# Performance work log

Measured on AMD Instinct MI355X. Metric: run time of the kernel, lower is better.

Reference implementation:

```python
import jax, jax.numpy as jnp
import numpy as np


def setup_inputs() -> dict:
    key = jax.random.key(0)
    k1, k2, k3 = jax.random.split(key, 3)
    n, num_dim, classes = 65536, 1024, 1000
    inputs = jax.random.normal(k1, (n, num_dim), dtype=jnp.float32)
    targets = jax.random.randint(k2, (n,), 0, classes, dtype=jnp.int64)
    class_weight = jax.random.normal(k3, (classes, num_dim), dtype=jnp.float32)
    return {"inputs": inputs, "targets": targets, "classes": classes, "class_weight": class_weight}


def reference(inputs, targets, classes, class_weight):
    # Per-class mean (segment mean) for classes present in the batch;
    # absent classes fall back to the corresponding class_weight row.
    sums = jax.ops.segment_sum(inputs, targets, num_segments=classes)  # [classes, dim]
    counts = jax.ops.segment_sum(jnp.ones((inputs.shape[0],), inputs.dtype), targets, num_segments=classes)  # [classes]
    present = counts > 0
    means = sums / jnp.maximum(counts, 1.0)[:, None]
    centers = jnp.where(present[:, None], means, class_weight)
    return centers
```

## Files before the change

### kernel.cpp

```cpp
#include <hip/hip_runtime.h>


typedef float floatx4 __attribute__((ext_vector_type(4)));

__global__ void zero_kernel(int* __restrict__ p, int n) {
    int i = blockIdx.x * blockDim.x + threadIdx.x;
    if (i < n) p[i] = 0;
}

__global__ void count_kernel(const int* __restrict__ targets, int* __restrict__ counts, int n) {
    int i = blockIdx.x * blockDim.x + threadIdx.x;
    if (i < n) atomicAdd(&counts[targets[i]], 1);
}

__global__ void scan_kernel(const int* __restrict__ counts, int* __restrict__ offsets, int c) {
    __shared__ int buf[2][1024];
    int tid = threadIdx.x;
    int v = (tid < c) ? counts[tid] : 0;
    buf[0][tid] = v;
    __syncthreads();
    int src = 0;
    for (int d = 1; d < 1024; d <<= 1) {
        int x = buf[src][tid];
        if (tid >= d) x += buf[src][tid - d];
        buf[src ^ 1][tid] = x;
        src ^= 1;
        __syncthreads();
    }
    if (tid < c) offsets[tid] = buf[src][tid] - v;
}

__global__ void scatter_kernel(const int* __restrict__ targets,
                               const int* __restrict__ offsets,
                               int* __restrict__ cursors,
                               int* __restrict__ binned, int n) {
    int i = blockIdx.x * blockDim.x + threadIdx.x;
    if (i < n) {
        int t = targets[i];
        int pos = atomicAdd(&cursors[t], 1);
        binned[offsets[t] + pos] = i;
    }
}

__global__ void gather_kernel(const floatx4* __restrict__ in4,
                              const int* __restrict__ counts,
                              const int* __restrict__ offsets,
                              const int* __restrict__ binned,
                              floatx4* __restrict__ part4, int d4) {
    int b = blockIdx.x;
    int c = b >> 1, half = b & 1;
    int cnt = counts[c];
    if (cnt == 0) return;
    int mid = (cnt + 1) >> 1;
    int begin = half ? mid : 0;
    int end   = half ? cnt : mid;
    int off = offsets[c] + begin;
    int m = end - begin;
    int tid = threadIdx.x;

    __shared__ int rows[1024];
    floatx4 a0 = {0,0,0,0}, a1 = {0,0,0,0}, a2 = {0,0,0,0}, a3 = {0,0,0,0};
    floatx4 a4 = {0,0,0,0}, a5 = {0,0,0,0}, a6 = {0,0,0,0}, a7 = {0,0,0,0};

    for (int base = 0; base < m; base += 1024) {
        int mm = min(m - base, 1024);
        __syncthreads();
        for (int j = tid; j < mm; j += blockDim.x) rows[j] = binned[off + base + j];
        __syncthreads();
        int j = 0;
        for (; j + 7 < mm; j += 8) {
            int r0 = rows[j],   r1 = rows[j+1], r2 = rows[j+2], r3 = rows[j+3];
            int r4 = rows[j+4], r5 = rows[j+5], r6 = rows[j+6], r7 = rows[j+7];
            a0 += __builtin_nontemporal_load(&in4[(size_t)r0 * d4 + tid]);
            a1 += __builtin_nontemporal_load(&in4[(size_t)r1 * d4 + tid]);
            a2 += __builtin_nontemporal_load(&in4[(size_t)r2 * d4 + tid]);
            a3 += __builtin_nontemporal_load(&in4[(size_t)r3 * d4 + tid]);
            a4 += __builtin_nontemporal_load(&in4[(size_t)r4 * d4 + tid]);
            a5 += __builtin_nontemporal_load(&in4[(size_t)r5 * d4 + tid]);
            a6 += __builtin_nontemporal_load(&in4[(size_t)r6 * d4 + tid]);
            a7 += __builtin_nontemporal_load(&in4[(size_t)r7 * d4 + tid]);
        }
        for (; j < mm; ++j)
            a0 += __builtin_nontemporal_load(&in4[(size_t)rows[j] * d4 + tid]);
    }
    floatx4 s = ((a0 + a1) + (a2 + a3)) + ((a4 + a5) + (a6 + a7));
    part4[(size_t)b * d4 + tid] = s;
}

__global__ void finalize_kernel(const floatx4* __restrict__ part4,
                                const floatx4* __restrict__ w4,
                                const int* __restrict__ counts,
                                floatx4* __restrict__ out4, int d4) {
    int c = blockIdx.x;
    int tid = threadIdx.x;
    int cnt = counts[c];
    size_t o = (size_t)c * d4 + tid;
    floatx4 r;
    if (cnt > 0) {
        floatx4 s = part4[(size_t)(c << 1) * d4 + tid]
                  + part4[(size_t)((c << 1) | 1) * d4 + tid];
        r = s * (1.0f / (float)cnt);
    } else {
        r = w4[o];
    }
    out4[o] = r;
}

extern "C" void kernel_launch(void* const* d_in, const int* in_sizes, int n_in,
                              void* d_out, int out_size, void* d_ws, size_t ws_size,
                              hipStream_t stream) {
    const float* inputs = (const float*)d_in[0];
    const int* targets  = (const int*)d_in[1];
    const float* weight = (const float*)d_in[3];

    const int N = in_sizes[1];
    const int D = in_sizes[0] / N;
    const int C = in_sizes[3] / D;
    const int D4 = D / 4;

    int* counts  = (int*)d_ws;
    int* cursors = counts + C;
    int* offsets = cursors + C;
    int* binned  = offsets + C;
    float* part  = (float*)(binned + N);

    zero_kernel<<<(2 * C + 255) / 256, 256, 0, stream>>>(counts, 2 * C);

    count_kernel<<<(N + 255) / 256, 256, 0, stream>>>(targets, counts, N);

    scan_kernel<<<1, 1024, 0, stream>>>(counts, offsets, C);

    scatter_kernel<<<(N + 255) / 256, 256, 0, stream>>>(targets, offsets, cursors, binned, N);

    gather_kernel<<<2 * C, D4, 0, stream>>>(
        (const floatx4*)inputs, counts, offsets, binned, (floatx4*)part, D4);

    finalize_kernel<<<C, D4, 0, stream>>>(
        (const floatx4*)part, (const floatx4*)weight, counts, (floatx4*)d_out, D4);
}
```

Before: 391.5 us.

## Fuse histogram and scan into one block, split gather into four per class

Replaces the zero, count and scan kernels with a single one-block kernel that builds the class histogram in shared memory, scans it, and writes the counts, offsets and starting cursors. The scatter kernel now writes directly at an atomically advanced cursor. The gather splits each class across four blocks instead of two to raise parallelism, and it uses normal loads instead of nontemporal ones. The single-block histogram serializes a pass over 65536 targets on one CU, which adds latency that may offset the two launches it removes.

```diff
diff --git a/kernel.cpp b/kernel.cpp
--- a/kernel.cpp
+++ b/kernel.cpp
@@ -3,20 +3,20 @@
 
 typedef float floatx4 __attribute__((ext_vector_type(4)));
 
-__global__ void zero_kernel(int* __restrict__ p, int n) {
-    int i = blockIdx.x * blockDim.x + threadIdx.x;
-    if (i < n) p[i] = 0;
-}
+#define SPLIT 4
 
-__global__ void count_kernel(const int* __restrict__ targets, int* __restrict__ counts, int n) {
-    int i = blockIdx.x * blockDim.x + threadIdx.x;
-    if (i < n) atomicAdd(&counts[targets[i]], 1);
-}
-
-__global__ void scan_kernel(const int* __restrict__ counts, int* __restrict__ offsets, int c) {
+__global__ void hist_scan_kernel(const int* __restrict__ targets, int n, int c,
+                                 int* __restrict__ counts,
+                                 int* __restrict__ offsets,
+                                 int* __restrict__ cursors) {
+    __shared__ int h[1024];
     __shared__ int buf[2][1024];
     int tid = threadIdx.x;
-    int v = (tid < c) ? counts[tid] : 0;
+    h[tid] = 0;
+    __syncthreads();
+    for (int i = tid; i < n; i += 1024) atomicAdd(&h[targets[i]], 1);
+    __syncthreads();
+    int v = h[tid];
     buf[0][tid] = v;
     __syncthreads();
     int src = 0;
@@ -27,18 +27,21 @@
         src ^= 1;
         __syncthreads();
     }
-    if (tid < c) offsets[tid] = buf[src][tid] - v;
+    if (tid < c) {
+        int excl = buf[src][tid] - v;
+        counts[tid]  = v;
+        offsets[tid] = excl;
+        cursors[tid] = excl;
+    }
 }
 
 __global__ void scatter_kernel(const int* __restrict__ targets,
-                               const int* __restrict__ offsets,
                                int* __restrict__ cursors,
                                int* __restrict__ binned, int n) {
     int i = blockIdx.x * blockDim.x + threadIdx.x;
     if (i < n) {
-        int t = targets[i];
-        int pos = atomicAdd(&cursors[t], 1);
-        binned[offsets[t] + pos] = i;
+        int pos = atomicAdd(&cursors[targets[i]], 1);
+        binned[pos] = i;
     }
 }
 
@@ -48,12 +51,11 @@
                               const int* __restrict__ binned,
                               floatx4* __restrict__ part4, int d4) {
     int b = blockIdx.x;
-    int c = b >> 1, half = b & 1;
+    int c = b >> 2, q = b & 3;
     int cnt = counts[c];
     if (cnt == 0) return;
-    int mid = (cnt + 1) >> 1;
-    int begin = half ? mid : 0;
-    int end   = half ? cnt : mid;
+    int begin = (cnt * q) >> 2;
+    int end   = (cnt * (q + 1)) >> 2;
     int off = offsets[c] + begin;
     int m = end - begin;
     int tid = threadIdx.x;
@@ -71,17 +73,17 @@
         for (; j + 7 < mm; j += 8) {
             int r0 = rows[j],   r1 = rows[j+1], r2 = rows[j+2], r3 = rows[j+3];
             int r4 = rows[j+4], r5 = rows[j+5], r6 = rows[j+6], r7 = rows[j+7];
-            a0 += __builtin_nontemporal_load(&in4[(size_t)r0 * d4 + tid]);
-            a1 += __builtin_nontemporal_load(&in4[(size_t)r1 * d4 + tid]);
-            a2 += __builtin_nontemporal_load(&in4[(size_t)r2 * d4 + tid]);
-            a3 += __builtin_nontemporal_load(&in4[(size_t)r3 * d4 + tid]);
-            a4 += __builtin_nontemporal_load(&in4[(size_t)r4 * d4 + tid]);
-            a5 += __builtin_nontemporal_load(&in4[(size_t)r5 * d4 + tid]);
-            a6 += __builtin_nontemporal_load(&in4[(size_t)r6 * d4 + tid]);
-            a7 += __builtin_nontemporal_load(&in4[(size_t)r7 * d4 + tid]);
+            a0 += in4[(size_t)r0 * d4 + tid];
+            a1 += in4[(size_t)r1 * d4 + tid];
+            a2 += in4[(size_t)r2 * d4 + tid];
+            a3 += in4[(size_t)r3 * d4 + tid];
+            a4 += in4[(size_t)r4 * d4 + tid];
+            a5 += in4[(size_t)r5 * d4 + tid];
+            a6 += in4[(size_t)r6 * d4 + tid];
+            a7 += in4[(size_t)r7 * d4 + tid];
         }
         for (; j < mm; ++j)
-            a0 += __builtin_nontemporal_load(&in4[(size_t)rows[j] * d4 + tid]);
+            a0 += in4[(size_t)rows[j] * d4 + tid];
     }
     floatx4 s = ((a0 + a1) + (a2 + a3)) + ((a4 + a5) + (a6 + a7));
     part4[(size_t)b * d4 + tid] = s;
@@ -97,8 +99,9 @@
     size_t o = (size_t)c * d4 + tid;
     floatx4 r;
     if (cnt > 0) {
-        floatx4 s = part4[(size_t)(c << 1) * d4 + tid]
-                  + part4[(size_t)((c << 1) | 1) * d4 + tid];
+        size_t pb = (size_t)(c << 2) * d4 + tid;
+        floatx4 s = (part4[pb] + part4[pb + d4])
+                  + (part4[pb + 2 * d4] + part4[pb + 3 * d4]);
         r = s * (1.0f / (float)cnt);
     } else {
         r = w4[o];
@@ -124,15 +127,11 @@
     int* binned  = offsets + C;
     float* part  = (float*)(binned + N);
 
-    zero_kernel<<<(2 * C + 255) / 256, 256, 0, stream>>>(counts, 2 * C);
+    hist_scan_kernel<<<1, 1024, 0, stream>>>(targets, N, C, counts, offsets, cursors);
 
-    count_kernel<<<(N + 255) / 256, 256, 0, stream>>>(targets, counts, N);
+    scatter_kernel<<<(N + 255) / 256, 256, 0, stream>>>(targets, cursors, binned, N);
 
-    scan_kernel<<<1, 1024, 0, stream>>>(counts, offsets, C);
-
-    scatter_kernel<<<(N + 255) / 256, 256, 0, stream>>>(targets, offsets, cursors, binned, N);
-
-    gather_kernel<<<2 * C, D4, 0, stream>>>(
+    gather_kernel<<<SPLIT * C, D4, 0, stream>>>(
         (const floatx4*)inputs, counts, offsets, binned, (floatx4*)part, D4);
 
     finalize_kernel<<<C, D4, 0, stream>>>(
```

Measured after the change: 421.0 us. 1.08x slower.
